# Kernel optimization log

Hardware: AMD Instinct MI355X
Metric: run time of the kernel (lower is better)

## Reference

```python
import jax, jax.numpy as jnp
import numpy as np

B, C, H, W = 128, 3, 256, 256
STEPS = 64
T_MIN, T_MAX = 0.02, 0.98
RES = (T_MAX - T_MIN) / (STEPS - 1)


def setup_inputs() -> dict:
    key = jax.random.key(0)
    x = jax.random.uniform(key, (B, C, H, W), dtype=jnp.float32)
    return {"x": x}


def _cell_filtrations(V):
    # V-construction cubical complex (sublevel): vertex cells carry pixel values,
    # edge cells carry max of their 2 endpoint vertices, square cells max of 4 corners.
    Eh = jnp.maximum(V[..., :, :-1], V[..., :, 1:])          # [.., H,   W-1] horizontal edges (dim 1)
    Ev = jnp.maximum(V[..., :-1, :], V[..., 1:, :])          # [.., H-1, W  ] vertical edges (dim 1)
    S = jnp.maximum(jnp.maximum(V[..., :-1, :-1], V[..., :-1, 1:]),
                    jnp.maximum(V[..., 1:, :-1], V[..., 1:, 1:]))  # [.., H-1, W-1] squares (dim 2)
    return Eh, Ev, S


def _bins(f):
    # t = max(ceil((filt - t_min)/resolution), 0); cells with filt > t_max are masked out.
    return jnp.clip(jnp.ceil((f - T_MIN) / RES).astype(jnp.int32), 0, STEPS - 1)


def reference(x):
    b, c = x.shape[0], x.shape[1]
    V = x  # sublevel filtration
    Eh, Ev, S = _cell_filtrations(V)
    filts = jnp.concatenate([V.reshape(b, c, -1), Eh.reshape(b, c, -1),
                             Ev.reshape(b, c, -1), S.reshape(b, c, -1)], axis=-1)
    n_v = H * W
    n_eh = H * (W - 1)
    n_ev = (H - 1) * W
    n_s = (H - 1) * (W - 1)
    # Euler characteristic signs (-1)**dim per cell type.
    signs = jnp.concatenate([jnp.ones(n_v, jnp.float32), -jnp.ones(n_eh, jnp.float32),
                             -jnp.ones(n_ev, jnp.float32), jnp.ones(n_s, jnp.float32)])
    t = _bins(filts)                                   # [B, C, N] bin index per cell
    contrib = signs * (filts <= T_MAX).astype(jnp.float32)

    def one_image(tb, cb):
        ecc = jnp.zeros(STEPS, jnp.float32).at[tb].add(cb)
        return jnp.cumsum(ecc)

    return jax.vmap(jax.vmap(one_image))(t, contrib)   # [B, C, STEPS]
```

## Files before the change

kernel.cpp:

```cpp
#include <hip/hip_runtime.h>

#define IMG_H 256
#define IMG_W 256
#define BAND  32
#define NBANDS (IMG_H / BAND)
#define NIMG  (128 * 3)
#define STEPS 64

__device__ __forceinline__ int bin_of(float v) {
    const float T_MIN = 0.02f;
    const float RES_F = (float)(0.96 / 63.0);
    int t = (int)ceilf((v - T_MIN) / RES_F);
    t = t < 0 ? 0 : t;
    return t > 63 ? 63 : t;
}

__global__ __launch_bounds__(256) void ecc_main(const float* __restrict__ x,
                                                int* __restrict__ hist) {
    const int img  = blockIdx.x / NBANDS;
    const int band = blockIdx.x % NBANDS;
    const int j    = threadIdx.x;
    const int wave = j >> 6;

    __shared__ float rows[BAND + 2][IMG_W + 2];
    __shared__ int   lh[4][STEPS];

    ((int*)lh)[threadIdx.x] = 0;

    const float* base = x + (size_t)img * (IMG_H * IMG_W);
    const int r0 = band * BAND - 1;
#pragma unroll
    for (int k = 0; k < BAND + 2; ++k) {
        int r = r0 + k;
        float v = (r >= 0 && r < IMG_H) ? base[r * IMG_W + j] : 1e30f;
        rows[k][j + 1] = v;
    }
    if (j < BAND + 2) { rows[j][0] = 1e30f; rows[j][IMG_W + 1] = 1e30f; }
    __syncthreads();

    float ul = rows[0][j], u = rows[0][j + 1], ur = rows[0][j + 2];
    float l  = rows[1][j], c = rows[1][j + 1], r  = rows[1][j + 2];

    for (int k = 0; k < BAND; ++k) {
        float dl = rows[k + 2][j], d = rows[k + 2][j + 1], dr = rows[k + 2][j + 2];
        if (c <= 0.98f) {
            bool oR = (r  < c);
            bool oL = (l <= c);
            bool oD = (d  < c);
            bool oU = (u <= c);
            bool sDR = oR & oD & (dr <  c);
            bool sDL = oL & oD & (dl <  c);
            bool sUR = oU & oR & (ur <= c);
            bool sUL = oU & oL & (ul <= c);
            int contrib = 1 - ((int)oR + (int)oL + (int)oD + (int)oU)
                            + ((int)sDR + (int)sDL + (int)sUR + (int)sUL);
            if (contrib != 0) atomicAdd(&lh[wave][bin_of(c)], contrib);
        }
        ul = l; u = c; ur = r;
        l = dl; c = d; r = dr;
    }
    __syncthreads();

    if (threadIdx.x < STEPS) {
        int t = threadIdx.x;
        int tot = lh[0][t] + lh[1][t] + lh[2][t] + lh[3][t];
        if (tot) atomicAdd(&hist[img * STEPS + t], tot);
    }
}

__global__ __launch_bounds__(64) void ecc_scan(const int* __restrict__ hist,
                                               float* __restrict__ out) {
    const int img = blockIdx.x;
    const int t   = threadIdx.x;
    int v = hist[img * STEPS + t];
#pragma unroll
    for (int d = 1; d < 64; d <<= 1) {
        int y = __shfl_up(v, d, 64);
        if (t >= d) v += y;
    }
    out[img * STEPS + t] = (float)v;
}

extern "C" void kernel_launch(void* const* d_in, const int* in_sizes, int n_in,
                              void* d_out, int out_size, void* d_ws, size_t ws_size,
                              hipStream_t stream) {
    const float* x = (const float*)d_in[0];
    float* out = (float*)d_out;
    int* hist = (int*)d_ws;

    hipMemsetAsync(hist, 0, (size_t)NIMG * STEPS * sizeof(int), stream);
    ecc_main<<<dim3(NIMG * NBANDS), dim3(256), 0, stream>>>(x, hist);
    ecc_scan<<<dim3(NIMG), dim3(64), 0, stream>>>(hist, out);
}
```

Before: 159.2 us.

## Replace shared-memory row staging with per-thread float4 register strips

```diff
diff --git a/kernel.cpp b/kernel.cpp
--- a/kernel.cpp
+++ b/kernel.cpp
@@ -1,11 +1,13 @@
 #include <hip/hip_runtime.h>
 
-#define IMG_H 256
-#define IMG_W 256
-#define BAND  32
-#define NBANDS (IMG_H / BAND)
-#define NIMG  (128 * 3)
-#define STEPS 64
+#define IMG     256
+#define NIMG    384
+#define STEPS   64
+#define ROWS_PT 16
+#define STRIPS  4
+#define ROWS_PB (ROWS_PT * STRIPS)
+#define BANDS   (IMG / ROWS_PB)
+#define INFV    1e30f
 
 __device__ __forceinline__ int bin_of(float v) {
     const float T_MIN = 0.02f;
@@ -15,52 +17,62 @@
     return t > 63 ? 63 : t;
 }
 
+__device__ __forceinline__ void load_row(const float* __restrict__ base,
+                                         int r, int col0, float w[6]) {
+    if ((unsigned)r >= IMG) {
+        w[0] = w[1] = w[2] = w[3] = w[4] = w[5] = INFV;
+        return;
+    }
+    const float* p = base + r * IMG + col0;
+    float4 q = *(const float4*)p;
+    w[1] = q.x; w[2] = q.y; w[3] = q.z; w[4] = q.w;
+    w[0] = (col0 > 0)       ? p[-1] : INFV;
+    w[5] = (col0 + 4 < IMG) ? p[4]  : INFV;
+}
+
 __global__ __launch_bounds__(256) void ecc_main(const float* __restrict__ x,
                                                 int* __restrict__ hist) {
-    const int img  = blockIdx.x / NBANDS;
-    const int band = blockIdx.x % NBANDS;
-    const int j    = threadIdx.x;
-    const int wave = j >> 6;
+    const int img   = blockIdx.x / BANDS;
+    const int band  = blockIdx.x % BANDS;
+    const int lane  = threadIdx.x & 63;
+    const int strip = threadIdx.x >> 6;
+    const int col0  = lane * 4;
+    const int r0    = band * ROWS_PB + strip * ROWS_PT;
 
-    __shared__ float rows[BAND + 2][IMG_W + 2];
-    __shared__ int   lh[4][STEPS];
-
+    __shared__ int lh[STRIPS][STEPS];
     ((int*)lh)[threadIdx.x] = 0;
-
-    const float* base = x + (size_t)img * (IMG_H * IMG_W);
-    const int r0 = band * BAND - 1;
-#pragma unroll
-    for (int k = 0; k < BAND + 2; ++k) {
-        int r = r0 + k;
-        float v = (r >= 0 && r < IMG_H) ? base[r * IMG_W + j] : 1e30f;
-        rows[k][j + 1] = v;
-    }
-    if (j < BAND + 2) { rows[j][0] = 1e30f; rows[j][IMG_W + 1] = 1e30f; }
     __syncthreads();
 
-    float ul = rows[0][j], u = rows[0][j + 1], ur = rows[0][j + 2];
-    float l  = rows[1][j], c = rows[1][j + 1], r  = rows[1][j + 2];
+    const float* base = x + (size_t)img * (IMG * IMG);
 
-    for (int k = 0; k < BAND; ++k) {
-        float dl = rows[k + 2][j], d = rows[k + 2][j + 1], dr = rows[k + 2][j + 2];
-        if (c <= 0.98f) {
-            bool oR = (r  < c);
-            bool oL = (l <= c);
-            bool oD = (d  < c);
-            bool oU = (u <= c);
-            bool sDR = oR & oD & (dr <  c);
-            bool sDL = oL & oD & (dl <  c);
-            bool sUR = oU & oR & (ur <= c);
-            bool sUL = oU & oL & (ul <= c);
-            int contrib = 1 - ((int)oR + (int)oL + (int)oD + (int)oU)
-                            + ((int)sDR + (int)sDL + (int)sUR + (int)sUL);
-            if (contrib != 0) atomicAdd(&lh[wave][bin_of(c)], contrib);
+    float u[6], c[6], d[6];
+    load_row(base, r0 - 1, col0, u);
+    load_row(base, r0,     col0, c);
+
+    for (int k = 0; k < ROWS_PT; ++k) {
+        load_row(base, r0 + k + 1, col0, d);
+#pragma unroll
+        for (int i = 1; i <= 4; ++i) {
+            float cv = c[i];
+            if (cv <= 0.98f) {
+                bool oR = (c[i + 1] <  cv);
+                bool oL = (c[i - 1] <= cv);
+                bool oD = (d[i]     <  cv);
+                bool oU = (u[i]     <= cv);
+                bool sDR = oR & oD & (d[i + 1] <  cv);
+                bool sDL = oL & oD & (d[i - 1] <  cv);
+                bool sUR = oU & oR & (u[i + 1] <= cv);
+                bool sUL = oU & oL & (u[i - 1] <= cv);
+                int contrib = 1 - ((int)oR + (int)oL + (int)oD + (int)oU)
+                                + ((int)sDR + (int)sDL + (int)sUR + (int)sUL);
+                if (contrib) atomicAdd(&lh[strip][bin_of(cv)], contrib);
+            }
         }
-        ul = l; u = c; ur = r;
-        l = dl; c = d; r = dr;
+#pragma unroll
+        for (int i = 0; i < 6; ++i) { u[i] = c[i]; c[i] = d[i]; }
     }
+
     __syncthreads();
-
     if (threadIdx.x < STEPS) {
         int t = threadIdx.x;
         int tot = lh[0][t] + lh[1][t] + lh[2][t] + lh[3][t];
@@ -74,9 +86,9 @@
     const int t   = threadIdx.x;
     int v = hist[img * STEPS + t];
 #pragma unroll
-    for (int d = 1; d < 64; d <<= 1) {
-        int y = __shfl_up(v, d, 64);
-        if (t >= d) v += y;
+    for (int s = 1; s < 64; s <<= 1) {
+        int y = __shfl_up(v, s, 64);
+        if (t >= s) v += y;
     }
     out[img * STEPS + t] = (float)v;
 }
@@ -89,6 +101,6 @@
     int* hist = (int*)d_ws;
 
     hipMemsetAsync(hist, 0, (size_t)NIMG * STEPS * sizeof(int), stream);
-    ecc_main<<<dim3(NIMG * NBANDS), dim3(256), 0, stream>>>(x, hist);
+    ecc_main<<<dim3(NIMG * BANDS), dim3(256), 0, stream>>>(x, hist);
     ecc_scan<<<dim3(NIMG), dim3(64), 0, stream>>>(hist, out);
 }
```

Result: no change. 158.3 us (-0.6%).
